# Kernel optimization log

Hardware: AMD Instinct MI355X
Metric: run time of the kernel (lower is better)

Reference implementation:

```python
import jax, jax.numpy as jnp
import numpy as np

B, S, D, H = 2, 2048, 4096, 32
Dh = D // H          # 128, rotary_dim == head_dim
BASE = 10000.0       # rope_theta
SCALE = Dh ** -0.5


def setup_inputs() -> dict:
    key = jax.random.key(0)
    k0, k1, k2 = jax.random.split(key, 3)
    w_scale = 0.02
    return {
        "hidden_states": jax.random.normal(k0, (B, S, D), jnp.float32),
        "positions": jnp.broadcast_to(jnp.arange(S, dtype=jnp.int32), (B, S)),
        "Wqkv": jax.random.normal(k1, (D, 3 * D), jnp.float32) * w_scale,
        "bqkv": jnp.zeros((3 * D,), jnp.float32),
        "Wproj": jax.random.normal(k2, (D, D), jnp.float32) * w_scale,
    }


def _apply_rope(x, positions):
    # x: [B, S, H, Dh]; neox-style (rotate-half) RoPE, as in vLLM PagedAttentionWithRoPE
    half = Dh // 2
    inv_freq = 1.0 / (BASE ** (jnp.arange(half, dtype=jnp.float32) / half))
    ang = positions[..., None].astype(jnp.float32) * inv_freq      # [B, S, half]
    cos = jnp.cos(ang)[:, :, None, :]                              # [B, S, 1, half]
    sin = jnp.sin(ang)[:, :, None, :]
    x1, x2 = x[..., :half], x[..., half:]
    return jnp.concatenate([x1 * cos - x2 * sin, x2 * cos + x1 * sin], axis=-1)


def reference(hidden_states, positions, Wqkv, bqkv, Wproj):
    # c_attn: fused QKV projection
    qkv = hidden_states @ Wqkv + bqkv                              # [B, S, 3D]
    q, k, v = jnp.split(qkv, 3, axis=-1)
    q = q.reshape(B, S, H, Dh)
    k = k.reshape(B, S, H, Dh)
    v = v.reshape(B, S, H, Dh)
    # fused RoPE on q and k at the given positions
    q = _apply_rope(q, positions)
    k = _apply_rope(k, positions)
    # causal scaled-dot-product attention (prefill semantics of paged attention)
    scores = jnp.einsum("bqhd,bkhd->bhqk", q, k) * SCALE           # [B, H, S, S]
    causal = jnp.tril(jnp.ones((S, S), dtype=bool))
    scores = jnp.where(causal, scores, jnp.finfo(scores.dtype).min)
    attn = jax.nn.softmax(scores, axis=-1)
    ctx = jnp.einsum("bhqk,bkhd->bqhd", attn, v).reshape(B, S, D)
    # c_proj (no bias)
    return ctx @ Wproj
```

## Files before the change

kernel.cpp:

```cpp
#include <hip/hip_runtime.h>

typedef __attribute__((ext_vector_type(8))) short short8;
typedef __attribute__((ext_vector_type(4))) short short4v;
typedef __attribute__((ext_vector_type(4))) float f32x4;

#define LDS8(base, off) (*(const short8*)((const char*)(base) + (off)))
#define GLOAD_LDS16(gp, lp) __builtin_amdgcn_global_load_lds( \
    (const __attribute__((address_space(1))) unsigned int*)(gp), \
    (__attribute__((address_space(3))) unsigned int*)(lp), 16, 0, 0)
#define BARRIER() asm volatile("s_barrier" ::: "memory")

__device__ __forceinline__ short f2bf(float f) {
    unsigned u = __builtin_bit_cast(unsigned, f);
    unsigned r = (u + 0x7FFFu + ((u >> 16) & 1u)) >> 16;
    return (short)r;
}
__device__ __forceinline__ float bf2f(short s) {
    unsigned u = ((unsigned)(unsigned short)s) << 16;
    return __builtin_bit_cast(float, u);
}

__global__ __launch_bounds__(256) void cvt_f32_bf16(const float* __restrict__ in,
                                                    short* __restrict__ out, int n8) {
    int i = blockIdx.x * 256 + threadIdx.x;
    if (i < n8) {
        const f32x4* p = (const f32x4*)(in + (size_t)i * 8);
        f32x4 a = p[0], bq = p[1];
        short8 o;
        o[0] = f2bf(a[0]); o[1] = f2bf(a[1]); o[2] = f2bf(a[2]); o[3] = f2bf(a[3]);
        o[4] = f2bf(bq[0]); o[5] = f2bf(bq[1]); o[6] = f2bf(bq[2]); o[7] = f2bf(bq[3]);
        *(short8*)(out + (size_t)i * 8) = o;
    }
}

__global__ __launch_bounds__(256) void transpose_cvt(const float* __restrict__ W,
                                                     short* __restrict__ Out, int R, int C) {
    __shared__ float tile[64][33];
    int c0 = blockIdx.x * 64, r0 = blockIdx.y * 32;
    int tid = threadIdx.x;
    int cc4 = (tid & 15) * 4;
#pragma unroll
    for (int it = 0; it < 2; ++it) {
        int rr = (tid >> 4) + it * 16;
        f32x4 v = *(const f32x4*)&W[(size_t)(r0 + rr) * C + c0 + cc4];
#pragma unroll
        for (int i = 0; i < 4; ++i) tile[cc4 + i][rr] = v[i];
    }
    __syncthreads();
    int cc = tid >> 2, r8 = (tid & 3) * 8;
    short8 o;
#pragma unroll
    for (int i = 0; i < 8; ++i) o[i] = f2bf(tile[cc][r8 + i]);
    *(short8*)&Out[(size_t)(c0 + cc) * R + r0 + r8] = o;
}

__global__ __launch_bounds__(256) void rope_table(float* __restrict__ ctab, float* __restrict__ stab) {
    int idx = blockIdx.x * 256 + threadIdx.x;
    int t = idx >> 6, j = idx & 63;
    float inv = expf(-(float)j * (9.210340371976184f / 64.0f));
    float ang = (float)t * inv;
    ctab[idx] = cosf(ang);
    stab[idx] = sinf(ang);
}

__global__ __launch_bounds__(256) void rope_scatter(const short* __restrict__ qkv,
                                                    const int* __restrict__ pos,
                                                    const float* __restrict__ ctab,
                                                    const float* __restrict__ stab,
                                                    short* __restrict__ Q, short* __restrict__ K) {
    int id = blockIdx.x * 256 + threadIdx.x;
    int j = id & 63;
    int h = (id >> 6) & 31;
    int s = (id >> 11) & 2047;
    int b = id >> 22;
    size_t qrow = (size_t)(b * 2048 + s) * 12288 + h * 128;
    float q1 = bf2f(qkv[qrow + j]),        q2 = bf2f(qkv[qrow + 64 + j]);
    float k1 = bf2f(qkv[qrow + 4096 + j]), k2 = bf2f(qkv[qrow + 4160 + j]);
    int p = pos[b * 2048 + s];
    float c = ctab[p * 64 + j], si = stab[p * 64 + j];
    size_t orow = ((size_t)(b * 32 + h) * 2048 + s) * 128;
    Q[orow + j]      = f2bf(q1 * c - q2 * si);
    Q[orow + 64 + j] = f2bf(q2 * c + q1 * si);
    K[orow + j]      = f2bf(k1 * c - k2 * si);
    K[orow + 64 + j] = f2bf(k2 * c + k1 * si);
}

__global__ __launch_bounds__(256) void v_transpose(const short* __restrict__ qkv,
                                                   short* __restrict__ Vt) {
    int bh = blockIdx.z; int b = bh >> 5, h = bh & 31;
    int d0 = blockIdx.x * 32, s0 = blockIdx.y * 32;
    __shared__ short tile[32][33];
    int tx = threadIdx.x & 31, ty = threadIdx.x >> 5;
#pragma unroll
    for (int i = 0; i < 4; ++i) {
        int sr = ty * 4 + i;
        tile[sr][tx] = qkv[(size_t)(b * 2048 + s0 + sr) * 12288 + 8192 + h * 128 + d0 + tx];
    }
    __syncthreads();
#pragma unroll
    for (int i = 0; i < 4; ++i) {
        int dr = ty * 4 + i;
        Vt[((size_t)bh * 128 + d0 + dr) * 2048 + s0 + tx] = tile[tx][dr];
    }
}

__global__ __launch_bounds__(512, 2) void gemm256(const short* __restrict__ A,
                                                  const short* __restrict__ Bt,
                                                  const float* __restrict__ bias,
                                                  short* __restrict__ Cbf,
                                                  float* __restrict__ Cf,
                                                  int M, int N, int K, int nN) {
    __shared__ __align__(16) char smem[131072];
    const int tid = threadIdx.x;
    const int l = tid & 63, w = tid >> 6;
    const int m = l & 15, g = l >> 4, m7 = m & 7;
    const int wm = w >> 2, wn = w & 3;

    int cpx = gridDim.x >> 3;
    int wg = (blockIdx.x & 7) * cpx + (blockIdx.x >> 3);
    int bm = wg / nN, bn = wg - bm * nN;
    int m0 = bm << 8, n0 = bn << 8;

    const int srow = l >> 3;
    const int sgcol = ((l & 7) ^ srow) << 3;

    const int NT = K >> 6;

    const int AbaseR = wm << 14;
    const int BbaseR = 32768 + ((wn >> 1) << 14);
    const int brow0 = (wn & 1) << 6;

    f32x4 acc[8][4];
    const f32x4 fz = {0.f, 0.f, 0.f, 0.f};
#pragma unroll
    for (int i = 0; i < 8; ++i)
#pragma unroll
        for (int j = 0; j < 4; ++j) acc[i][j] = fz;

    auto stage_half = [&](const short* G, int grow0, int kcol, int ldsoff) {
        GLOAD_LDS16(G + (size_t)(grow0 +      w * 8 + srow) * K + kcol + sgcol,
                    smem + ldsoff + w * 1024);
        GLOAD_LDS16(G + (size_t)(grow0 + 64 + w * 8 + srow) * K + kcol + sgcol,
                    smem + ldsoff + 8192 + w * 1024);
    };

    short8 af[2][2], bf[4][2];

#define RD_A(I0)                                                                 \
    _Pragma("unroll")                                                            \
    for (int i2 = 0; i2 < 2; ++i2) {                                             \
        _Pragma("unroll")                                                        \
        for (int kk = 0; kk < 2; ++kk)                                           \
            af[i2][kk] = LDS8(Ab, (((I0) + i2) * 16 + m) * 128 + (((kk * 4 + g) ^ m7) << 4)); \
    }

#define MFMA_IP(IP)                                                              \
    do {                                                                         \
        __builtin_amdgcn_s_setprio(1);                                           \
        _Pragma("unroll")                                                        \
        for (int i2 = 0; i2 < 2; ++i2) {                                         \
            _Pragma("unroll")                                                    \
            for (int j2 = 0; j2 < 4; ++j2) {                                     \
                _Pragma("unroll")                                                \
                for (int kk = 0; kk < 2; ++kk) {                                 \
                    acc[(IP) * 2 + i2][j2] = __builtin_amdgcn_mfma_f32_16x16x32_bf16( \
                        af[i2][kk], bf[j2][kk], acc[(IP) * 2 + i2][j2], 0, 0, 0); \
                }                                                                \
            }                                                                    \
        }                                                                        \
        __builtin_amdgcn_s_setprio(0);                                           \
    } while (0)

#pragma unroll
    for (int t = 0; t < 2; ++t) {
        int sb = t << 16;
        stage_half(A,  m0,       t * 64, sb);
        stage_half(A,  m0 + 128, t * 64, sb + 16384);
        stage_half(Bt, n0,       t * 64, sb + 32768);
        stage_half(Bt, n0 + 128, t * 64, sb + 49152);
    }
    asm volatile("s_waitcnt vmcnt(8)" ::: "memory");
    __builtin_amdgcn_sched_barrier(0);
    BARRIER();

    for (int kt = 0; kt < NT; ++kt) {
        const int slotb = (kt & 1) << 16;
        const char* Ab = smem + slotb + AbaseR;
        const char* Bb = smem + slotb + BbaseR;
        const bool pf = (kt + 2) < NT;
        const int kc = (kt + 2) << 6;

#pragma unroll
        for (int j = 0; j < 4; ++j) {
#pragma unroll
            for (int kk = 0; kk < 2; ++kk)
                bf[j][kk] = LDS8(Bb, (brow0 + j * 16 + m) * 128 + (((kk * 4 + g) ^ m7) << 4));
        }
        RD_A(0);
        asm volatile("s_waitcnt lgkmcnt(8)" ::: "memory");
        BARRIER();
        MFMA_IP(0);
        BARRIER();

        RD_A(2);
        if (pf) stage_half(Bt, n0, kc, slotb + 32768);
        BARRIER();
        MFMA_IP(1);
        BARRIER();

        RD_A(4);
        if (pf) stage_half(Bt, n0 + 128, kc, slotb + 49152);
        BARRIER();
        MFMA_IP(2);
        BARRIER();

        RD_A(6);
        BARRIER();
        MFMA_IP(3);
        if (pf) {
            stage_half(A, m0,       kc, slotb);
            stage_half(A, m0 + 128, kc, slotb + 16384);
        }
        if (kt == NT - 2)     asm volatile("s_waitcnt vmcnt(0)" ::: "memory");
        else if (kt < NT - 1) asm volatile("s_waitcnt vmcnt(6)" ::: "memory");
        BARRIER();
    }
#undef RD_A
#undef MFMA_IP

#pragma unroll
    for (int i = 0; i < 8; ++i) {
#pragma unroll
        for (int j = 0; j < 4; ++j) {
#pragma unroll
            for (int r = 0; r < 4; ++r) {
                int row = m0 + wm * 128 + i * 16 + g * 4 + r;
                int col = n0 + wn * 64 + j * 16 + m;
                float v = acc[i][j][r];
                if (bias) v += bias[col];
                if (Cbf) Cbf[(size_t)row * N + col] = f2bf(v);
                else     Cf[(size_t)row * N + col] = v;
            }
        }
    }
}

__global__ __launch_bounds__(512, 4) void flash_fwd(const short* __restrict__ Q,
                                                    const short* __restrict__ Kt,
                                                    const short* __restrict__ Vt,
                                                    short* __restrict__ ctx) {
    const int S = 2048;
    const float SCALE = 0.08838834764831845f;
    __shared__ __align__(16) char smem[81920];

    int tid = threadIdx.x, l = tid & 63, w = tid >> 6;
    int m = l & 15, g = l >> 4, m7 = m & 7;
    int qg = blockIdx.x, h = blockIdx.y, b = blockIdx.z;
    int bh = b * 32 + h;
    int q0 = qg * 128 + w * 16;

    const short* Qg = Q + ((size_t)bh * S + q0) * 128;
    const short* Kg = Kt + (size_t)bh * S * 128;
    const short* Vg = Vt + (size_t)bh * 128 * S;

    short8 qf[4];
#pragma unroll
    for (int kb = 0; kb < 4; ++kb)
        qf[kb] = *(const short8*)(Qg + m * 128 + kb * 32 + g * 8);

    const f32x4 fz = {0.f, 0.f, 0.f, 0.f};
    f32x4 O[8];
#pragma unroll
    for (int nb = 0; nb < 8; ++nb) O[nb] = fz;
    float Mr[4], Lr[4];
#pragma unroll
    for (int r = 0; r < 4; ++r) { Mr[r] = -__builtin_inff(); Lr[r] = 0.f; }

    const short* Kp[2]; const short* Vp[2]; int KlO[2], VlO[2];
#pragma unroll
    for (int q = 0; q < 2; ++q) {
        int c = w * 2 + q;
        int rowK = c * 4 + (l >> 4);
        Kp[q] = Kg + (size_t)rowK * 128 + (((l & 15) ^ (rowK & 7)) * 8);
        KlO[q] = c * 1024;
        int rowV = c * 8 + (l >> 3);
        Vp[q] = Vg + (size_t)rowV * S + (((l & 7) ^ (rowV & 7)) * 8);
        VlO[q] = c * 1024;
    }

    auto stage = [&](int t, int slot) {
#pragma unroll
        for (int q = 0; q < 2; ++q) {
            GLOAD_LDS16(Kp[q] + (size_t)t * 8192, smem + slot * 16384 + KlO[q]);
            GLOAD_LDS16(Vp[q] + t * 64, smem + 32768 + slot * 16384 + VlO[q]);
        }
    };

    int nkt = 2 * qg + 2;
    stage(0, 0);
    asm volatile("s_waitcnt vmcnt(0)" ::: "memory");
    __builtin_amdgcn_sched_barrier(0);
    BARRIER();

    for (int kt = 0; kt < nkt; ++kt) {
        if (kt + 1 < nkt) stage(kt + 1, (kt + 1) & 1);
        const char* Kl = smem + (kt & 1) * 16384;
        const char* Vl = smem + 32768 + (kt & 1) * 16384;
        char* Pl = smem + 65536 + w * 2048;
        int k0 = kt * 64;
        if (k0 <= q0 + 15) {
            f32x4 sc[4];
#pragma unroll
            for (int j = 0; j < 4; ++j) sc[j] = fz;
#pragma unroll
            for (int kb = 0; kb < 4; ++kb) {
#pragma unroll
                for (int j = 0; j < 4; ++j) {
                    short8 kf = LDS8(Kl, (j * 16 + m) * 256 + (((kb * 4 + g) ^ m7) << 4));
                    sc[j] = __builtin_amdgcn_mfma_f32_16x16x32_bf16(qf[kb], kf, sc[j], 0, 0, 0);
                }
            }
            bool diag = (k0 + 63 > q0);
#pragma unroll
            for (int r = 0; r < 4; ++r) {
                int qrow = q0 + g * 4 + r;
                float s0 = sc[0][r] * SCALE;
                float s1 = sc[1][r] * SCALE;
                float s2 = sc[2][r] * SCALE;
                float s3 = sc[3][r] * SCALE;
                if (diag) {
                    if (k0 + m > qrow)      s0 = -__builtin_inff();
                    if (k0 + 16 + m > qrow) s1 = -__builtin_inff();
                    if (k0 + 32 + m > qrow) s2 = -__builtin_inff();
                    if (k0 + 48 + m > qrow) s3 = -__builtin_inff();
                }
                float mx = fmaxf(fmaxf(s0, s1), fmaxf(s2, s3));
                mx = fmaxf(mx, __shfl_xor(mx, 1, 64));
                mx = fmaxf(mx, __shfl_xor(mx, 2, 64));
                mx = fmaxf(mx, __shfl_xor(mx, 4, 64));
                mx = fmaxf(mx, __shfl_xor(mx, 8, 64));
                float mnew = fmaxf(Mr[r], mx);
                float alpha = __expf(Mr[r] - mnew);
                float p0 = __expf(s0 - mnew);
                float p1 = __expf(s1 - mnew);
                float p2 = __expf(s2 - mnew);
                float p3 = __expf(s3 - mnew);
                float rs = (p0 + p1) + (p2 + p3);
                rs += __shfl_xor(rs, 1, 64);
                rs += __shfl_xor(rs, 2, 64);
                rs += __shfl_xor(rs, 4, 64);
                rs += __shfl_xor(rs, 8, 64);
                Lr[r] = Lr[r] * alpha + rs;
                Mr[r] = mnew;
#pragma unroll
                for (int nb = 0; nb < 8; ++nb) O[nb][r] *= alpha;
                int pr = g * 4 + r;
                char* pw = Pl + pr * 128;
                float pv[4] = {p0, p1, p2, p3};
#pragma unroll
                for (int j = 0; j < 4; ++j) {
                    int lb = j * 32 + m * 2;
                    int pb = (((lb >> 4) ^ (pr & 7)) << 4) | (lb & 15);
                    *(short*)(pw + pb) = f2bf(pv[j]);
                }
            }
            short8 pf[2];
#pragma unroll
            for (int kh = 0; kh < 2; ++kh)
                pf[kh] = LDS8(Pl, m * 128 + (((kh * 4 + g) ^ m7) << 4));
#pragma unroll
            for (int nb = 0; nb < 8; ++nb) {
                int d = nb * 16 + m;
#pragma unroll
                for (int kh = 0; kh < 2; ++kh) {
                    short8 vf = LDS8(Vl, d * 128 + (((kh * 4 + g) ^ m7) << 4));
                    O[nb] = __builtin_amdgcn_mfma_f32_16x16x32_bf16(pf[kh], vf, O[nb], 0, 0, 0);
                }
            }
        }
        if (kt + 1 < nkt) {
            asm volatile("s_waitcnt vmcnt(0)" ::: "memory");
            BARRIER();
        }
    }
#pragma unroll
    for (int nb = 0; nb < 8; ++nb) {
#pragma unroll
        for (int r = 0; r < 4; ++r) {
            int row = q0 + g * 4 + r;
            float v = O[nb][r] / Lr[r];
            ctx[(size_t)(b * S + row) * 4096 + h * 128 + nb * 16 + m] = f2bf(v);
        }
    }
}

extern "C" void kernel_launch(void* const* d_in, const int* in_sizes, int n_in,
                              void* d_out, int out_size, void* d_ws, size_t ws_size,
                              hipStream_t stream) {
    const float* hidden    = (const float*)d_in[0];
    const int*   positions = (const int*)d_in[1];
    const float* Wqkv      = (const float*)d_in[2];
    const float* bqkv      = (const float*)d_in[3];
    const float* Wproj     = (const float*)d_in[4];
    float* out = (float*)d_out;
    char* ws = (char*)d_ws;

    short* Abf    = (short*)(ws + 0ull);
    short* WqkvT  = (short*)(ws + 33554432ull);
    short* WprojT = (short*)(ws + 134217728ull);
    short* qkv    = (short*)(ws + 167772160ull);
    short* Qr     = (short*)(ws + 268435456ull);
    short* Kr     = (short*)(ws + 301989888ull);
    short* Vt     = (short*)(ws + 335544320ull);
    short* ctx    = (short*)(ws + 369098752ull);
    float* ctab   = (float*)(ws + 402653184ull);
    float* stab   = (float*)(ws + 403177472ull);

    cvt_f32_bf16<<<8192, 256, 0, stream>>>(hidden, Abf, 2097152);
    transpose_cvt<<<dim3(192, 128), 256, 0, stream>>>(Wqkv, WqkvT, 4096, 12288);
    transpose_cvt<<<dim3(64, 128), 256, 0, stream>>>(Wproj, WprojT, 4096, 4096);
    rope_table<<<512, 256, 0, stream>>>(ctab, stab);
    gemm256<<<dim3(768), 512, 0, stream>>>(Abf, WqkvT, bqkv, qkv, nullptr, 4096, 12288, 4096, 48);
    rope_scatter<<<32768, 256, 0, stream>>>(qkv, positions, ctab, stab, Qr, Kr);
    v_transpose<<<dim3(4, 64, 64), 256, 0, stream>>>(qkv, Vt);
    flash_fwd<<<dim3(16, 32, 2), 512, 0, stream>>>(Qr, Kr, Vt, ctx);
    gemm256<<<dim3(256), 512, 0, stream>>>(ctx, WprojT, nullptr, nullptr, out, 4096, 4096, 4096, 16);
}
```

Measured before the change: 905.6 us.

## Software-pipeline LDS fragment reads across k-tiles with double-buffered B registers

Restructures the GEMM main loop so the A and B fragments for the next k-tile are read from LDS while the current tile's MFMAs run. B fragments are double-buffered in registers (bf0/bf1), the loop is unrolled by two, and global row pointers are precomputed once. The goal is to hide LDS read latency behind MFMA work and drop per-iteration address arithmetic. In exchange it raises register pressure and changes the vmcnt waits, which risks hazards or spills. It also assumes NT is even.

Result: slower. 1.261 ms (+39.3%).

```diff
diff --git a/kernel.cpp b/kernel.cpp
--- a/kernel.cpp
+++ b/kernel.cpp
@@ -123,8 +123,17 @@
 
     const int srow = l >> 3;
     const int sgcol = ((l & 7) ^ srow) << 3;
-
     const int NT = K >> 6;
+
+    const short* ApL0 = A  + (size_t)(m0 +       w * 8 + srow) * K + sgcol;
+    const short* ApL1 = A  + (size_t)(m0 +  64 + w * 8 + srow) * K + sgcol;
+    const short* ApH0 = A  + (size_t)(m0 + 128 + w * 8 + srow) * K + sgcol;
+    const short* ApH1 = A  + (size_t)(m0 + 192 + w * 8 + srow) * K + sgcol;
+    const short* BpL0 = Bt + (size_t)(n0 +       w * 8 + srow) * K + sgcol;
+    const short* BpL1 = Bt + (size_t)(n0 +  64 + w * 8 + srow) * K + sgcol;
+    const short* BpH0 = Bt + (size_t)(n0 + 128 + w * 8 + srow) * K + sgcol;
+    const short* BpH1 = Bt + (size_t)(n0 + 192 + w * 8 + srow) * K + sgcol;
+    const int w1k = w * 1024;
 
     const int AbaseR = wm << 14;
     const int BbaseR = 32768 + ((wn >> 1) << 14);
@@ -137,96 +146,112 @@
 #pragma unroll
         for (int j = 0; j < 4; ++j) acc[i][j] = fz;
 
-    auto stage_half = [&](const short* G, int grow0, int kcol, int ldsoff) {
-        GLOAD_LDS16(G + (size_t)(grow0 +      w * 8 + srow) * K + kcol + sgcol,
-                    smem + ldsoff + w * 1024);
-        GLOAD_LDS16(G + (size_t)(grow0 + 64 + w * 8 + srow) * K + kcol + sgcol,
-                    smem + ldsoff + 8192 + w * 1024);
-    };
-
-    short8 af[2][2], bf[4][2];
-
-#define RD_A(I0)                                                                 \
-    _Pragma("unroll")                                                            \
-    for (int i2 = 0; i2 < 2; ++i2) {                                             \
-        _Pragma("unroll")                                                        \
-        for (int kk = 0; kk < 2; ++kk)                                           \
-            af[i2][kk] = LDS8(Ab, (((I0) + i2) * 16 + m) * 128 + (((kk * 4 + g) ^ m7) << 4)); \
-    }
-
-#define MFMA_IP(IP)                                                              \
-    do {                                                                         \
-        __builtin_amdgcn_s_setprio(1);                                           \
-        _Pragma("unroll")                                                        \
-        for (int i2 = 0; i2 < 2; ++i2) {                                         \
-            _Pragma("unroll")                                                    \
-            for (int j2 = 0; j2 < 4; ++j2) {                                     \
-                _Pragma("unroll")                                                \
-                for (int kk = 0; kk < 2; ++kk) {                                 \
-                    acc[(IP) * 2 + i2][j2] = __builtin_amdgcn_mfma_f32_16x16x32_bf16( \
-                        af[i2][kk], bf[j2][kk], acc[(IP) * 2 + i2][j2], 0, 0, 0); \
-                }                                                                \
-            }                                                                    \
-        }                                                                        \
-        __builtin_amdgcn_s_setprio(0);                                           \
+    short8 afX[2][2], afY[2][2], bf0[4][2], bf1[4][2];
+
+#define RD_AF(DST, BASE, I0)                                                             \
+    _Pragma("unroll")                                                                    \
+    for (int i2 = 0; i2 < 2; ++i2) {                                                     \
+        _Pragma("unroll")                                                                \
+        for (int kk = 0; kk < 2; ++kk)                                                   \
+            DST[i2][kk] = LDS8(BASE, (((I0) + i2) * 16 + m) * 128 + (((kk * 4 + g) ^ m7) << 4)); \
+    }
+#define RD_BF2(DST, BASE, J0)                                                            \
+    _Pragma("unroll")                                                                    \
+    for (int j2 = 0; j2 < 2; ++j2) {                                                     \
+        _Pragma("unroll")                                                                \
+        for (int kk = 0; kk < 2; ++kk)                                                   \
+            DST[(J0) + j2][kk] = LDS8(BASE, (brow0 + ((J0) + j2) * 16 + m) * 128 + (((kk * 4 + g) ^ m7) << 4)); \
+    }
+#define MFMA8(I0, AF, BF)                                                                \
+    do {                                                                                 \
+        __builtin_amdgcn_s_setprio(1);                                                   \
+        _Pragma("unroll")                                                                \
+        for (int kk = 0; kk < 2; ++kk) {                                                 \
+            _Pragma("unroll")                                                            \
+            for (int i2 = 0; i2 < 2; ++i2) {                                             \
+                _Pragma("unroll")                                                        \
+                for (int j2 = 0; j2 < 4; ++j2) {                                         \
+                    acc[(I0) + i2][j2] = __builtin_amdgcn_mfma_f32_16x16x32_bf16(        \
+                        AF[i2][kk], BF[j2][kk], acc[(I0) + i2][j2], 0, 0, 0);            \
+                }                                                                        \
+            }                                                                            \
+        }                                                                                \
+        __builtin_amdgcn_s_setprio(0);                                                   \
     } while (0)
 
 #pragma unroll
     for (int t = 0; t < 2; ++t) {
         int sb = t << 16;
-        stage_half(A,  m0,       t * 64, sb);
-        stage_half(A,  m0 + 128, t * 64, sb + 16384);
-        stage_half(Bt, n0,       t * 64, sb + 32768);
-        stage_half(Bt, n0 + 128, t * 64, sb + 49152);
+        int kc = t * 64;
+        GLOAD_LDS16(ApL0 + kc, smem + sb +         w1k);
+        GLOAD_LDS16(ApL1 + kc, smem + sb +  8192 + w1k);
+        GLOAD_LDS16(ApH0 + kc, smem + sb + 16384 + w1k);
+        GLOAD_LDS16(ApH1 + kc, smem + sb + 24576 + w1k);
+        GLOAD_LDS16(BpL0 + kc, smem + sb + 32768 + w1k);
+        GLOAD_LDS16(BpL1 + kc, smem + sb + 40960 + w1k);
+        GLOAD_LDS16(BpH0 + kc, smem + sb + 49152 + w1k);
+        GLOAD_LDS16(BpH1 + kc, smem + sb + 57344 + w1k);
     }
     asm volatile("s_waitcnt vmcnt(8)" ::: "memory");
     __builtin_amdgcn_sched_barrier(0);
     BARRIER();
-
-    for (int kt = 0; kt < NT; ++kt) {
-        const int slotb = (kt & 1) << 16;
-        const char* Ab = smem + slotb + AbaseR;
-        const char* Bb = smem + slotb + BbaseR;
-        const bool pf = (kt + 2) < NT;
-        const int kc = (kt + 2) << 6;
-
-#pragma unroll
-        for (int j = 0; j < 4; ++j) {
-#pragma unroll
-            for (int kk = 0; kk < 2; ++kk)
-                bf[j][kk] = LDS8(Bb, (brow0 + j * 16 + m) * 128 + (((kk * 4 + g) ^ m7) << 4));
-        }
-        RD_A(0);
-        asm volatile("s_waitcnt lgkmcnt(8)" ::: "memory");
-        BARRIER();
-        MFMA_IP(0);
-        BARRIER();
-
-        RD_A(2);
-        if (pf) stage_half(Bt, n0, kc, slotb + 32768);
-        BARRIER();
-        MFMA_IP(1);
-        BARRIER();
-
-        RD_A(4);
-        if (pf) stage_half(Bt, n0 + 128, kc, slotb + 49152);
-        BARRIER();
-        MFMA_IP(2);
-        BARRIER();
-
-        RD_A(6);
-        BARRIER();
-        MFMA_IP(3);
-        if (pf) {
-            stage_half(A, m0,       kc, slotb);
-            stage_half(A, m0 + 128, kc, slotb + 16384);
-        }
-        if (kt == NT - 2)     asm volatile("s_waitcnt vmcnt(0)" ::: "memory");
-        else if (kt < NT - 1) asm volatile("s_waitcnt vmcnt(6)" ::: "memory");
-        BARRIER();
-    }
-#undef RD_A
-#undef MFMA_IP
+    {
+        const char* Ab0 = smem + AbaseR;
+        const char* Bb0 = smem + BbaseR;
+        RD_BF2(bf0, Bb0, 0);
+        RD_BF2(bf0, Bb0, 2);
+        RD_AF(afX, Ab0, 0);
+    }
+
+#define TILE_BODY(KT, CURBF, NXTBF)                                                      \
+    {                                                                                    \
+        const int slotb = ((KT) & 1) << 16;                                              \
+        const char* Ab  = smem + slotb + AbaseR;                                         \
+        const char* AbN = smem + (slotb ^ 65536) + AbaseR;                               \
+        const char* BbN = smem + (slotb ^ 65536) + BbaseR;                               \
+        const bool pf = (KT) + 2 < NT;                                                   \
+        const bool nx = (KT) + 1 < NT;                                                   \
+        const int kc = ((KT) + 2) << 6;                                                  \
+                                                                                \
+        RD_AF(afY, Ab, 2);                                                               \
+        BARRIER();                                                                       \
+        MFMA8(0, afX, CURBF);                                                            \
+        if (pf) { GLOAD_LDS16(BpL0 + kc, smem + slotb + 32768 + w1k);                    \
+                  GLOAD_LDS16(BpL1 + kc, smem + slotb + 40960 + w1k); }                  \
+        BARRIER();                                                                       \
+                                                                                \
+        RD_AF(afX, Ab, 4);                                                               \
+        BARRIER();                                                                       \
+        MFMA8(2, afY, CURBF);                                                            \
+        if (pf) { GLOAD_LDS16(BpH0 + kc, smem + slotb + 49152 + w1k);                    \
+                  GLOAD_LDS16(BpH1 + kc, smem + slotb + 57344 + w1k); }                  \
+        asm volatile("s_waitcnt vmcnt(4)" ::: "memory");                                 \
+        BARRIER();                                                                       \
+                                                                                \
+        RD_AF(afY, Ab, 6);                                                               \
+        if (nx) { RD_BF2(NXTBF, BbN, 0); }                                               \
+        BARRIER();                                                                       \
+        MFMA8(4, afX, CURBF);                                                            \
+        BARRIER();                                                                       \
+                                                                                \
+        if (nx) { RD_AF(afX, AbN, 0); RD_BF2(NXTBF, BbN, 2); }                           \
+        BARRIER();                                                                       \
+        MFMA8(6, afY, CURBF);                                                            \
+        if (pf) { GLOAD_LDS16(ApL0 + kc, smem + slotb +         w1k);                    \
+                  GLOAD_LDS16(ApL1 + kc, smem + slotb +  8192 + w1k);                    \
+                  GLOAD_LDS16(ApH0 + kc, smem + slotb + 16384 + w1k);                    \
+                  GLOAD_LDS16(ApH1 + kc, smem + slotb + 24576 + w1k); }                  \
+        BARRIER();                                                                       \
+    }
+
+    for (int kt = 0; kt < NT; kt += 2) {
+        TILE_BODY(kt,     bf0, bf1);
+        TILE_BODY(kt + 1, bf1, bf0);
+    }
+#undef TILE_BODY
+#undef RD_AF
+#undef RD_BF2
+#undef MFMA8
 
 #pragma unroll
     for (int i = 0; i < 8; ++i) {
```
